# Optimization experiments

Measured on AMD Instinct MI355X. Metric: run time of the kernel, lower is better.

The kernel has to match this reference:

```python
import jax, jax.numpy as jnp
import numpy as np

EPS = 1e-5

def _bn(x, w, b, rm, rv):
    # eval-mode BatchNorm over channel axis (x: [..., C] broadcastable)
    return (x - rm) * (w * jax.lax.rsqrt(rv + EPS)) + b

def setup_inputs() -> dict:
    key = jax.random.key(0)
    ks = jax.random.split(key, 20)
    B, C, H, W = 2, 64, 96, 96
    Cq = C // 8  # query/key channels
    Cr = C // 8  # SE reduction channels
    s = 0.05
    inp = {
        'x': jax.random.normal(ks[0], (B, C, H, W), jnp.float32),
        'wq': jax.random.normal(ks[1], (Cq, C), jnp.float32) * s,
        'bq': jnp.zeros((Cq,), jnp.float32),
        'wk': jax.random.normal(ks[2], (Cq, C), jnp.float32) * s,
        'bk': jnp.zeros((Cq,), jnp.float32),
        'wv': jax.random.normal(ks[3], (C, C), jnp.float32) * s,
        'bv': jnp.zeros((C,), jnp.float32),
        'gamma': jnp.full((1,), 0.5, jnp.float32),
        'bn_w': jnp.ones((C,), jnp.float32),
        'bn_b': jnp.zeros((C,), jnp.float32),
        'bn_rm': jax.random.normal(ks[4], (C,), jnp.float32) * 0.1,
        'bn_rv': jax.random.uniform(ks[5], (C,), jnp.float32) + 0.5,
        'se_w1': jax.random.normal(ks[6], (Cr, C), jnp.float32) * s,
        'se_b1': jnp.zeros((Cr,), jnp.float32),
        'se_bn1_w': jnp.ones((Cr,), jnp.float32),
        'se_bn1_b': jnp.zeros((Cr,), jnp.float32),
        'se_bn1_rm': jax.random.normal(ks[7], (Cr,), jnp.float32) * 0.1,
        'se_bn1_rv': jax.random.uniform(ks[8], (Cr,), jnp.float32) + 0.5,
        'se_w2': jax.random.normal(ks[9], (C, Cr), jnp.float32) * s,
        'se_b2': jnp.zeros((C,), jnp.float32),
        'se_bn2_w': jnp.ones((C,), jnp.float32),
        'se_bn2_b': jnp.zeros((C,), jnp.float32),
        'se_bn2_rm': jax.random.normal(ks[10], (C,), jnp.float32) * 0.1,
        'se_bn2_rv': jax.random.uniform(ks[11], (C,), jnp.float32) + 0.5,
    }
    return inp

def reference(x, wq, bq, wk, bk, wv, bv, gamma, bn_w, bn_b, bn_rm, bn_rv,
              se_w1, se_b1, se_bn1_w, se_bn1_b, se_bn1_rm, se_bn1_rv,
              se_w2, se_b2, se_bn2_w, se_bn2_b, se_bn2_rm, se_bn2_rv):
    B, C, H, W = x.shape
    N = H * W
    xf = x.reshape(B, C, N)
    # PAM branch: 1x1 conv projections
    q = jnp.einsum('oc,bcn->bno', wq, xf) + bq            # [B,N,C/8]
    k = jnp.einsum('oc,bcn->bon', wk, xf) + bk[:, None]    # [B,C/8,N]
    v = jnp.einsum('oc,bcn->bon', wv, xf) + bv[:, None]    # [B,C,N]
    energy = jnp.einsum('bno,bom->bnm', q, k)              # [B,N,N]
    attn = jax.nn.softmax(energy, axis=-1)
    # out[b,c,i] = sum_j v[b,c,j] * attn[b,i,j]  (bmm(V, attn^T))
    out = jnp.einsum('bcj,bij->bci', v, attn)
    out = gamma[0] * out
    out = _bn(out, bn_w[:, None], bn_b[:, None], bn_rm[:, None], bn_rv[:, None])
    pam = out.reshape(B, C, H, W)
    # SE branch: GAP + 1x1 conv-bn-relu x2, multiplicative gate
    a = xf.mean(axis=2)                                    # [B,C]
    a1 = jax.nn.relu(_bn(a @ se_w1.T + se_b1, se_bn1_w, se_bn1_b, se_bn1_rm, se_bn1_rv))
    a2 = jax.nn.relu(_bn(a1 @ se_w2.T + se_b2, se_bn2_w, se_bn2_b, se_bn2_rm, se_bn2_rv))
    se = x * a2[:, :, None, None]
    return x + se + pam
```

## Files before the change

### kernel.cpp

```cpp
#include <hip/hip_runtime.h>
#include <hip/hip_bf16.h>

#define B_SZ   2
#define C_CH   64
#define NQ     8
#define NPIX   9216
#define NJC    288
#define QBLKS  288
#define KPART  8
#define KEYS_P 1152
#define NCHUNK 18
#define SM_F   2080
#define NP4    2304
#define KSTEP  (64*NQ)
#define VSTEP  4096

typedef short bf16x8 __attribute__((ext_vector_type(8)));
typedef float f32x4  __attribute__((ext_vector_type(4)));
typedef unsigned u32x4 __attribute__((ext_vector_type(4)));
typedef unsigned uint2v __attribute__((ext_vector_type(2)));

static __device__ __forceinline__ unsigned pack2bf(float a, float b){
    unsigned r;
    asm("v_cvt_pk_bf16_f32 %0, %1, %2" : "=v"(r) : "v"(a), "v"(b));
    return r;
}

__global__ __launch_bounds__(256) void prep_kernel(
    const float* __restrict__ x,
    const float* __restrict__ wq, const float* __restrict__ bq,
    const float* __restrict__ wk, const float* __restrict__ bk,
    const float* __restrict__ wv, const float* __restrict__ bv,
    __hip_bfloat16* __restrict__ qp, __hip_bfloat16* __restrict__ kp,
    __hip_bfloat16* __restrict__ vswz, float* __restrict__ amean)
{
    const int blk = blockIdx.x, tid = threadIdx.x;
    if (blk < 144){
        int t  = blk*256 + tid;
        int n  = (t % NP4) * 4;
        int c8 = (t / NP4) & 7;
        int b  = t / (NP4*8);
        c8 = __builtin_amdgcn_readfirstlane(c8);
        b  = __builtin_amdgcn_readfirstlane(b);
        float acc[8][4];
#pragma unroll
        for (int k = 0; k < 8; ++k){
            float bvv = bv[c8*8 + k];
            acc[k][0] = bvv; acc[k][1] = bvv; acc[k][2] = bvv; acc[k][3] = bvv;
        }
#pragma unroll 4
        for (int ci = 0; ci < C_CH; ++ci){
            const float4 xv = *reinterpret_cast<const float4*>(
                x + (size_t)(b*C_CH + ci)*NPIX + n);
#pragma unroll
            for (int k = 0; k < 8; ++k){
                float w = wv[(c8*8 + k)*C_CH + ci];
                acc[k][0] = fmaf(xv.x, w, acc[k][0]);
                acc[k][1] = fmaf(xv.y, w, acc[k][1]);
                acc[k][2] = fmaf(xv.z, w, acc[k][2]);
                acc[k][3] = fmaf(xv.w, w, acc[k][3]);
            }
        }
#pragma unroll
        for (int k = 0; k < 8; ++k){
            int c = c8*8 + k;
            size_t base = ((size_t)((b*NJC + (n >> 5))*4 + (c >> 4)))*512
                        + ((c & 15)*32) + (n & 31);
            unsigned long long wpk =
                (unsigned long long)pack2bf(acc[k][0], acc[k][1]) |
                ((unsigned long long)pack2bf(acc[k][2], acc[k][3]) << 32);
            *reinterpret_cast<unsigned long long*>(vswz + base) = wpk;
        }
    } else if (blk < 180){
        int t  = (blk - 144)*256 + tid;
        int n  = (t % NP4) * 4;
        int o8 = (t / NP4) & 1;
        int b  = t / (NP4*2);
        o8 = __builtin_amdgcn_readfirstlane(o8);
        b  = __builtin_amdgcn_readfirstlane(b);
        const bool isq = (o8 == 0);
        const float* w    = isq ? wq : wk;
        const float* bias = isq ? bq : bk;
        float acc[8][4];
#pragma unroll
        for (int k = 0; k < 8; ++k){
            float bb = bias[k];
            acc[k][0] = bb; acc[k][1] = bb; acc[k][2] = bb; acc[k][3] = bb;
        }
#pragma unroll 4
        for (int ci = 0; ci < C_CH; ++ci){
            const float4 xv = *reinterpret_cast<const float4*>(
                x + (size_t)(b*C_CH + ci)*NPIX + n);
#pragma unroll
            for (int k = 0; k < 8; ++k){
                float wv_ = w[k*C_CH + ci];
                acc[k][0] = fmaf(xv.x, wv_, acc[k][0]);
                acc[k][1] = fmaf(xv.y, wv_, acc[k][1]);
                acc[k][2] = fmaf(xv.z, wv_, acc[k][2]);
                acc[k][3] = fmaf(xv.w, wv_, acc[k][3]);
            }
        }
        if (isq){
#pragma unroll
            for (int k = 0; k < 8; ++k)
#pragma unroll
                for (int px = 0; px < 4; ++px) acc[k][px] *= 1.44269504f;
        }
        __hip_bfloat16* dst = isq ? qp : kp;
#pragma unroll
        for (int px = 0; px < 4; ++px){
            u32x4 row;
            row[0] = pack2bf(acc[0][px], acc[1][px]);
            row[1] = pack2bf(acc[2][px], acc[3][px]);
            row[2] = pack2bf(acc[4][px], acc[5][px]);
            row[3] = pack2bf(acc[6][px], acc[7][px]);
            *reinterpret_cast<u32x4*>(dst + ((size_t)(b*NPIX + n + px))*NQ) = row;
        }
    } else {
        int bc = blk - 180;
        float s = 0.f;
        for (int i = tid; i < NPIX; i += 256) s += x[(size_t)bc*NPIX + i];
#pragma unroll
        for (int o = 32; o > 0; o >>= 1) s += __shfl_down(s, o, 64);
        __shared__ float red[4];
        if ((tid & 63) == 0) red[tid >> 6] = s;
        __syncthreads();
        if (tid == 0) amean[bc] = (red[0] + red[1] + red[2] + red[3]) * (1.f / (float)NPIX);
    }
}

__global__ __launch_bounds__(512, 2) void flash_fused(
    const __hip_bfloat16* __restrict__ qp,
    const __hip_bfloat16* __restrict__ kp,
    const __hip_bfloat16* __restrict__ vswz,
    const float* __restrict__ amean,
    const float* __restrict__ sw1, const float* __restrict__ sb1,
    const float* __restrict__ s1w, const float* __restrict__ s1b,
    const float* __restrict__ s1m, const float* __restrict__ s1v,
    const float* __restrict__ sw2, const float* __restrict__ sb2,
    const float* __restrict__ s2w, const float* __restrict__ s2b,
    const float* __restrict__ s2m, const float* __restrict__ s2v,
    const float* __restrict__ x,
    const float* __restrict__ gamma,
    const float* __restrict__ bnw, const float* __restrict__ bnb,
    const float* __restrict__ bnm, const float* __restrict__ bnv,
    float* __restrict__ out)
{
    __shared__ __align__(16) float sm[4*SM_F];

    const int qt2 = blockIdx.x, b = blockIdx.y;
    const int p  = threadIdx.x >> 6;
    const int l  = threadIdx.x & 63;
    const int lq = l & 15;
    const int lg = l >> 4;
    const int vlane = lq*32 + lg*8;

    bf16x8 zf = {0,0,0,0,0,0,0,0};
    bf16x8 qfrag[2];
#pragma unroll
    for (int qi = 0; qi < 2; ++qi){
        qfrag[qi] = zf;
        if (lg == 0)
            qfrag[qi] = *reinterpret_cast<const bf16x8*>(
                qp + (size_t)(b*NPIX + qt2*32 + qi*16 + lq) * NQ);
    }

    bf16x8 ones;
#pragma unroll
    for (int i = 0; i < 8; ++i) ones[i] = (short)0x3F80;

    f32x4 Of[2][4];
#pragma unroll
    for (int qi = 0; qi < 2; ++qi)
#pragma unroll
        for (int i = 0; i < 4; ++i) Of[qi][i] = (f32x4){0.f, 0.f, 0.f, 0.f};
    f32x4 Lf[2];
    Lf[0] = (f32x4){0.f, 0.f, 0.f, 0.f};
    Lf[1] = (f32x4){0.f, 0.f, 0.f, 0.f};

    const __hip_bfloat16* kptr = kp + ((size_t)(b*NPIX + p*KEYS_P + lq))*NQ;
    const __hip_bfloat16* vptr = vswz + ((size_t)(b*NJC + p*(KEYS_P/32)))*4*512 + vlane;

    bf16x8 kfa[4], vfa[2][4];
    bf16x8 kfb[4], vfb[2][4];

    auto loadK = [&](bf16x8 (&dst)[4], const __hip_bfloat16* ptr){
#pragma unroll
        for (int jt = 0; jt < 4; ++jt){
            dst[jt] = zf;
            if (lg == 0)
                dst[jt] = *reinterpret_cast<const bf16x8*>(ptr + jt*16*NQ);
        }
    };
    auto loadV = [&](bf16x8 (&dst)[2][4], const __hip_bfloat16* ptr){
#pragma unroll
        for (int kc = 0; kc < 2; ++kc)
#pragma unroll
            for (int ct = 0; ct < 4; ++ct)
                dst[kc][ct] = *reinterpret_cast<const bf16x8*>(ptr + (kc*4 + ct)*512);
    };
    auto compute = [&](bf16x8 (&kfc)[4], bf16x8 (&vfc)[2][4]){
#pragma unroll
        for (int qi = 0; qi < 2; ++qi){
            f32x4 Sf[4];
#pragma unroll
            for (int jt = 0; jt < 4; ++jt)
                Sf[jt] = __builtin_amdgcn_mfma_f32_16x16x32_bf16(kfc[jt], qfrag[qi], (f32x4){0.f,0.f,0.f,0.f}, 0, 0, 0);
            unsigned D[4][2];
#pragma unroll
            for (int jt = 0; jt < 4; ++jt){
                D[jt][0] = pack2bf(exp2f(Sf[jt][0]), exp2f(Sf[jt][1]));
                D[jt][1] = pack2bf(exp2f(Sf[jt][2]), exp2f(Sf[jt][3]));
            }
#pragma unroll
            for (int kc = 0; kc < 2; ++kc){
                unsigned o0, o1, o2, o3;
                {
                    uint2v r1 = __builtin_amdgcn_permlane32_swap(D[2*kc][0], D[2*kc+1][0], false, false);
                    uint2v r2 = __builtin_amdgcn_permlane16_swap(r1[0], r1[1], false, false);
                    o0 = r2[0]; o2 = r2[1];
                }
                {
                    uint2v r1 = __builtin_amdgcn_permlane32_swap(D[2*kc][1], D[2*kc+1][1], false, false);
                    uint2v r2 = __builtin_amdgcn_permlane16_swap(r1[0], r1[1], false, false);
                    o1 = r2[0]; o3 = r2[1];
                }
                u32x4 pu; pu[0] = o0; pu[1] = o1; pu[2] = o2; pu[3] = o3;
                bf16x8 pf = __builtin_bit_cast(bf16x8, pu);
#pragma unroll
                for (int ct = 0; ct < 4; ++ct)
                    Of[qi][ct] = __builtin_amdgcn_mfma_f32_16x16x32_bf16(vfc[kc][ct], pf, Of[qi][ct], 0, 0, 0);
                Lf[qi] = __builtin_amdgcn_mfma_f32_16x16x32_bf16(ones, pf, Lf[qi], 0, 0, 0);
            }
        }
    };

    loadK(kfa, kptr); loadV(vfa, vptr);
    kptr += KSTEP; vptr += VSTEP;

    for (int it = 0; it < (NCHUNK - 2)/2; ++it){
        loadK(kfb, kptr); loadV(vfb, vptr);
        kptr += KSTEP; vptr += VSTEP;
        compute(kfa, vfa);
        loadK(kfa, kptr); loadV(vfa, vptr);
        kptr += KSTEP; vptr += VSTEP;
        compute(kfb, vfb);
    }
    loadK(kfb, kptr); loadV(vfb, vptr);
    compute(kfa, vfa);
    compute(kfb, vfb);

    float a1r;
    {
        int r8 = l & 7;
        float s = sb1[r8];
#pragma unroll 8
        for (int c = 0; c < C_CH; ++c)
            s = fmaf(amean[b*C_CH + c], sw1[r8*C_CH + c], s);
        s = (s - s1m[r8]) * (s1w[r8] * rsqrtf(s1v[r8] + 1e-5f)) + s1b[r8];
        a1r = fmaxf(s, 0.f);
    }

    if (p >= 4){
        const int ps = p - 4;
#pragma unroll
        for (int qi = 0; qi < 2; ++qi)
#pragma unroll
            for (int ct = 0; ct < 4; ++ct)
#pragma unroll
                for (int r = 0; r < 4; ++r)
                    sm[ps*SM_F + qi*1024 + (ct*4 + r)*64 + l] = Of[qi][ct][r];
        if (l < 16){
            sm[ps*SM_F + 2048 + lq]      = Lf[0][0];
            sm[ps*SM_F + 2048 + 16 + lq] = Lf[1][0];
        }
    }
    __syncthreads();
    if (p < 4){
#pragma unroll
        for (int qi = 0; qi < 2; ++qi)
#pragma unroll
            for (int ct = 0; ct < 4; ++ct)
#pragma unroll
                for (int r = 0; r < 4; ++r)
                    sm[p*SM_F + qi*1024 + (ct*4 + r)*64 + l] += Of[qi][ct][r];
        if (l < 16){
            sm[p*SM_F + 2048 + lq]      += Lf[0][0];
            sm[p*SM_F + 2048 + 16 + lq] += Lf[1][0];
        }
    }
    __syncthreads();

    {
        const int w8 = threadIdx.x >> 6;
        const int qi = w8 >> 2;
        const int ct = w8 & 3;
        float gam = gamma[0];

        float a1g[8];
#pragma unroll
        for (int j = 0; j < 8; ++j) a1g[j] = __shfl(a1r, (l & 56) | j, 64);
        float a2v[4];
#pragma unroll
        for (int r = 0; r < 4; ++r){
            int c = ct*16 + lg*4 + r;
            float s = sb2[c];
#pragma unroll
            for (int j = 0; j < 8; ++j) s = fmaf(a1g[j], sw2[c*NQ + j], s);
            s = (s - s2m[c]) * (s2w[c] * rsqrtf(s2v[c] + 1e-5f)) + s2b[c];
            a2v[r] = fmaxf(s, 0.f);
        }

        float L = 0.f;
#pragma unroll
        for (int q = 0; q < 4; ++q) L += sm[q*SM_F + 2048 + qi*16 + lq];
        float invL = 1.f / L;
        int n = qt2*32 + qi*16 + lq;
#pragma unroll
        for (int r = 0; r < 4; ++r){
            float O = 0.f;
#pragma unroll
            for (int q = 0; q < 4; ++q) O += sm[q*SM_F + qi*1024 + (ct*4 + r)*64 + l];
            int c = ct*16 + lg*4 + r;
            float pam = gam * O * invL;
            pam = (pam - bnm[c]) * (bnw[c] * rsqrtf(bnv[c] + 1e-5f)) + bnb[c];
            float xv = x[(size_t)(b*C_CH + c)*NPIX + n];
            out[(size_t)(b*C_CH + c)*NPIX + n] = fmaf(xv, a2v[r], xv + pam);
        }
    }
}

extern "C" void kernel_launch(void* const* d_in, const int* in_sizes, int n_in,
                              void* d_out, int out_size, void* d_ws, size_t ws_size,
                              hipStream_t stream)
{
    const float* x     = (const float*)d_in[0];
    const float* wq    = (const float*)d_in[1];
    const float* bq    = (const float*)d_in[2];
    const float* wk    = (const float*)d_in[3];
    const float* bk    = (const float*)d_in[4];
    const float* wv    = (const float*)d_in[5];
    const float* bv    = (const float*)d_in[6];
    const float* gamma = (const float*)d_in[7];
    const float* bnw   = (const float*)d_in[8];
    const float* bnb   = (const float*)d_in[9];
    const float* bnm   = (const float*)d_in[10];
    const float* bnv   = (const float*)d_in[11];
    const float* sw1   = (const float*)d_in[12];
    const float* sb1   = (const float*)d_in[13];
    const float* s1w   = (const float*)d_in[14];
    const float* s1b   = (const float*)d_in[15];
    const float* s1m   = (const float*)d_in[16];
    const float* s1v   = (const float*)d_in[17];
    const float* sw2   = (const float*)d_in[18];
    const float* sb2   = (const float*)d_in[19];
    const float* s2w   = (const float*)d_in[20];
    const float* s2b   = (const float*)d_in[21];
    const float* s2m   = (const float*)d_in[22];
    const float* s2v   = (const float*)d_in[23];

    size_t off = 0;
    auto give = [&](size_t bytes) -> void* {
        void* r = (char*)d_ws + off;
        off += (bytes + 255) & ~(size_t)255;
        return r;
    };
    __hip_bfloat16* qp   = (__hip_bfloat16*)give((size_t)B_SZ*NPIX*NQ*2);
    __hip_bfloat16* kp   = (__hip_bfloat16*)give((size_t)B_SZ*NPIX*NQ*2);
    __hip_bfloat16* vswz = (__hip_bfloat16*)give((size_t)B_SZ*C_CH*NPIX*2);
    float* amean = (float*)give((size_t)B_SZ*C_CH*4);

    prep_kernel<<<dim3(308), dim3(256), 0, stream>>>(x, wq, bq, wk, bk, wv, bv,
                                                     qp, kp, vswz, amean);
    flash_fused<<<dim3(QBLKS, B_SZ), dim3(512), 0, stream>>>(
        qp, kp, vswz, amean,
        sw1, sb1, s1w, s1b, s1m, s1v,
        sw2, sb2, s2w, s2b, s2m, s2v,
        x, gamma, bnw, bnb, bnm, bnv, (float*)d_out);
}
```

Before: 204.6 us.

## Switch flash attention to 32x32x16 MFMA with repacked K/V layouts

Replaces the 16x16x32 bf16 MFMA tiles in the fused attention kernel with 32x32x16 tiles. Q/K rows are padded to 16 channels with zeros, and V is reswizzled into 16-key by 32-channel blocks to match the new operand layout. A single permlane32 swap now replaces the permlane32+permlane16 pair, and the epilogue remaps LDS indices to the new accumulator layout. The K/V register double-buffering is simplified to prefetching only K while V is loaded inside each chunk. The launch bound of 2 blocks per CU is dropped. The intent is fewer MFMA issues and less wasted zero-padding per lane, at the cost of doubled Q/K storage, possible occupancy change and less V prefetch overlap.

Result: faster. 192.9 us (-5.8%).

```diff
diff --git a/kernel.cpp b/kernel.cpp
--- a/kernel.cpp
+++ b/kernel.cpp
@@ -4,19 +4,21 @@
 #define B_SZ   2
 #define C_CH   64
 #define NQ     8
+#define QKS    16
 #define NPIX   9216
-#define NJC    288
+#define NKS    576
 #define QBLKS  288
 #define KPART  8
 #define KEYS_P 1152
 #define NCHUNK 18
 #define SM_F   2080
 #define NP4    2304
-#define KSTEP  (64*NQ)
+#define KSTEP2 1024
 #define VSTEP  4096
 
 typedef short bf16x8 __attribute__((ext_vector_type(8)));
 typedef float f32x4  __attribute__((ext_vector_type(4)));
+typedef float f32x16 __attribute__((ext_vector_type(16)));
 typedef unsigned u32x4 __attribute__((ext_vector_type(4)));
 typedef unsigned uint2v __attribute__((ext_vector_type(2)));
 
@@ -64,8 +66,8 @@
 #pragma unroll
         for (int k = 0; k < 8; ++k){
             int c = c8*8 + k;
-            size_t base = ((size_t)((b*NJC + (n >> 5))*4 + (c >> 4)))*512
-                        + ((c & 15)*32) + (n & 31);
+            size_t base = ((size_t)((b*NKS + (n >> 4))*2 + (c >> 5)))*512
+                        + (((n >> 3) & 1) << 8) + ((c & 31) << 3) + (n & 7);
             unsigned long long wpk =
                 (unsigned long long)pack2bf(acc[k][0], acc[k][1]) |
                 ((unsigned long long)pack2bf(acc[k][2], acc[k][3]) << 32);
@@ -107,6 +109,7 @@
                 for (int px = 0; px < 4; ++px) acc[k][px] *= 1.44269504f;
         }
         __hip_bfloat16* dst = isq ? qp : kp;
+        u32x4 zr; zr[0] = 0; zr[1] = 0; zr[2] = 0; zr[3] = 0;
 #pragma unroll
         for (int px = 0; px < 4; ++px){
             u32x4 row;
@@ -114,7 +117,9 @@
             row[1] = pack2bf(acc[2][px], acc[3][px]);
             row[2] = pack2bf(acc[4][px], acc[5][px]);
             row[3] = pack2bf(acc[6][px], acc[7][px]);
-            *reinterpret_cast<u32x4*>(dst + ((size_t)(b*NPIX + n + px))*NQ) = row;
+            __hip_bfloat16* d0 = dst + ((size_t)(b*NPIX + n + px))*QKS;
+            *reinterpret_cast<u32x4*>(d0)     = row;
+            *reinterpret_cast<u32x4*>(d0 + 8) = zr;
         }
     } else {
         int bc = blk - 180;
@@ -129,7 +134,7 @@
     }
 }
 
-__global__ __launch_bounds__(512, 2) void flash_fused(
+__global__ __launch_bounds__(512) void flash_fused(
     const __hip_bfloat16* __restrict__ qp,
     const __hip_bfloat16* __restrict__ kp,
     const __hip_bfloat16* __restrict__ vswz,
@@ -151,104 +156,77 @@
     const int qt2 = blockIdx.x, b = blockIdx.y;
     const int p  = threadIdx.x >> 6;
     const int l  = threadIdx.x & 63;
-    const int lq = l & 15;
-    const int lg = l >> 4;
-    const int vlane = lq*32 + lg*8;
-
-    bf16x8 zf = {0,0,0,0,0,0,0,0};
-    bf16x8 qfrag[2];
-#pragma unroll
-    for (int qi = 0; qi < 2; ++qi){
-        qfrag[qi] = zf;
-        if (lg == 0)
-            qfrag[qi] = *reinterpret_cast<const bf16x8*>(
-                qp + (size_t)(b*NPIX + qt2*32 + qi*16 + lq) * NQ);
-    }
+    const int lc = l & 31;
+    const int lh = l >> 5;
+
+    bf16x8 qfrag = *reinterpret_cast<const bf16x8*>(
+        qp + ((size_t)(b*NPIX + qt2*32 + lc))*QKS + lh*8);
 
     bf16x8 ones;
 #pragma unroll
     for (int i = 0; i < 8; ++i) ones[i] = (short)0x3F80;
 
-    f32x4 Of[2][4];
-#pragma unroll
-    for (int qi = 0; qi < 2; ++qi)
-#pragma unroll
-        for (int i = 0; i < 4; ++i) Of[qi][i] = (f32x4){0.f, 0.f, 0.f, 0.f};
-    f32x4 Lf[2];
-    Lf[0] = (f32x4){0.f, 0.f, 0.f, 0.f};
-    Lf[1] = (f32x4){0.f, 0.f, 0.f, 0.f};
-
-    const __hip_bfloat16* kptr = kp + ((size_t)(b*NPIX + p*KEYS_P + lq))*NQ;
-    const __hip_bfloat16* vptr = vswz + ((size_t)(b*NJC + p*(KEYS_P/32)))*4*512 + vlane;
-
-    bf16x8 kfa[4], vfa[2][4];
-    bf16x8 kfb[4], vfb[2][4];
-
-    auto loadK = [&](bf16x8 (&dst)[4], const __hip_bfloat16* ptr){
-#pragma unroll
-        for (int jt = 0; jt < 4; ++jt){
-            dst[jt] = zf;
-            if (lg == 0)
-                dst[jt] = *reinterpret_cast<const bf16x8*>(ptr + jt*16*NQ);
+    f32x16 zero16;
+#pragma unroll
+    for (int i = 0; i < 16; ++i) zero16[i] = 0.f;
+
+    f32x16 Of0 = zero16, Of1 = zero16;
+    f32x16 Lacc = zero16;
+
+    const __hip_bfloat16* kptr = kp + ((size_t)(b*NPIX + p*KEYS_P + lc))*QKS + lh*8;
+    const __hip_bfloat16* vptr = vswz + ((size_t)((b*NKS + p*(KEYS_P/16))*2))*512 + l*8;
+
+    auto CHUNK = [&](const bf16x8& k0, const bf16x8& k1){
+        bf16x8 vf[8];
+#pragma unroll
+        for (int t = 0; t < 8; ++t)
+            vf[t] = *reinterpret_cast<const bf16x8*>(vptr + t*512);
+        vptr += VSTEP;
+
+        unsigned D[16];
+#pragma unroll
+        for (int kt = 0; kt < 2; ++kt){
+            f32x16 s = __builtin_amdgcn_mfma_f32_32x32x16_bf16(
+                kt ? k1 : k0, qfrag, zero16, 0, 0, 0);
+#pragma unroll
+            for (int g = 0; g < 4; ++g){
+                float e0 = exp2f(s[4*g+0]), e1 = exp2f(s[4*g+1]);
+                float e2 = exp2f(s[4*g+2]), e3 = exp2f(s[4*g+3]);
+                D[kt*8 + g*2 + 0] = pack2bf(e0, e1);
+                D[kt*8 + g*2 + 1] = pack2bf(e2, e3);
+            }
+        }
+#pragma unroll
+        for (int ks = 0; ks < 4; ++ks){
+            const int base = (ks >> 1)*8 + (ks & 1)*4;
+            uint2v r0 = __builtin_amdgcn_permlane32_swap(D[base+0], D[base+2], false, false);
+            uint2v r1 = __builtin_amdgcn_permlane32_swap(D[base+1], D[base+3], false, false);
+            u32x4 pu; pu[0] = r0[0]; pu[1] = r1[0]; pu[2] = r0[1]; pu[3] = r1[1];
+            bf16x8 pf = __builtin_bit_cast(bf16x8, pu);
+            Of0  = __builtin_amdgcn_mfma_f32_32x32x16_bf16(vf[ks*2+0], pf, Of0, 0, 0, 0);
+            Of1  = __builtin_amdgcn_mfma_f32_32x32x16_bf16(vf[ks*2+1], pf, Of1, 0, 0, 0);
+            Lacc = __builtin_amdgcn_mfma_f32_32x32x16_bf16(ones,       pf, Lacc, 0, 0, 0);
         }
     };
-    auto loadV = [&](bf16x8 (&dst)[2][4], const __hip_bfloat16* ptr){
-#pragma unroll
-        for (int kc = 0; kc < 2; ++kc)
-#pragma unroll
-            for (int ct = 0; ct < 4; ++ct)
-                dst[kc][ct] = *reinterpret_cast<const bf16x8*>(ptr + (kc*4 + ct)*512);
-    };
-    auto compute = [&](bf16x8 (&kfc)[4], bf16x8 (&vfc)[2][4]){
-#pragma unroll
-        for (int qi = 0; qi < 2; ++qi){
-            f32x4 Sf[4];
-#pragma unroll
-            for (int jt = 0; jt < 4; ++jt)
-                Sf[jt] = __builtin_amdgcn_mfma_f32_16x16x32_bf16(kfc[jt], qfrag[qi], (f32x4){0.f,0.f,0.f,0.f}, 0, 0, 0);
-            unsigned D[4][2];
-#pragma unroll
-            for (int jt = 0; jt < 4; ++jt){
-                D[jt][0] = pack2bf(exp2f(Sf[jt][0]), exp2f(Sf[jt][1]));
-                D[jt][1] = pack2bf(exp2f(Sf[jt][2]), exp2f(Sf[jt][3]));
-            }
-#pragma unroll
-            for (int kc = 0; kc < 2; ++kc){
-                unsigned o0, o1, o2, o3;
-                {
-                    uint2v r1 = __builtin_amdgcn_permlane32_swap(D[2*kc][0], D[2*kc+1][0], false, false);
-                    uint2v r2 = __builtin_amdgcn_permlane16_swap(r1[0], r1[1], false, false);
-                    o0 = r2[0]; o2 = r2[1];
-                }
-                {
-                    uint2v r1 = __builtin_amdgcn_permlane32_swap(D[2*kc][1], D[2*kc+1][1], false, false);
-                    uint2v r2 = __builtin_amdgcn_permlane16_swap(r1[0], r1[1], false, false);
-                    o1 = r2[0]; o3 = r2[1];
-                }
-                u32x4 pu; pu[0] = o0; pu[1] = o1; pu[2] = o2; pu[3] = o3;
-                bf16x8 pf = __builtin_bit_cast(bf16x8, pu);
-#pragma unroll
-                for (int ct = 0; ct < 4; ++ct)
-                    Of[qi][ct] = __builtin_amdgcn_mfma_f32_16x16x32_bf16(vfc[kc][ct], pf, Of[qi][ct], 0, 0, 0);
-                Lf[qi] = __builtin_amdgcn_mfma_f32_16x16x32_bf16(ones, pf, Lf[qi], 0, 0, 0);
-            }
-        }
-    };
-
-    loadK(kfa, kptr); loadV(vfa, vptr);
-    kptr += KSTEP; vptr += VSTEP;
-
+
+    bf16x8 kA0 = *reinterpret_cast<const bf16x8*>(kptr);
+    bf16x8 kA1 = *reinterpret_cast<const bf16x8*>(kptr + 512);
+    kptr += KSTEP2;
+    bf16x8 kB0, kB1;
     for (int it = 0; it < (NCHUNK - 2)/2; ++it){
-        loadK(kfb, kptr); loadV(vfb, vptr);
-        kptr += KSTEP; vptr += VSTEP;
-        compute(kfa, vfa);
-        loadK(kfa, kptr); loadV(vfa, vptr);
-        kptr += KSTEP; vptr += VSTEP;
-        compute(kfb, vfb);
-    }
-    loadK(kfb, kptr); loadV(vfb, vptr);
-    compute(kfa, vfa);
-    compute(kfb, vfb);
+        kB0 = *reinterpret_cast<const bf16x8*>(kptr);
+        kB1 = *reinterpret_cast<const bf16x8*>(kptr + 512);
+        kptr += KSTEP2;
+        CHUNK(kA0, kA1);
+        kA0 = *reinterpret_cast<const bf16x8*>(kptr);
+        kA1 = *reinterpret_cast<const bf16x8*>(kptr + 512);
+        kptr += KSTEP2;
+        CHUNK(kB0, kB1);
+    }
+    kB0 = *reinterpret_cast<const bf16x8*>(kptr);
+    kB1 = *reinterpret_cast<const bf16x8*>(kptr + 512);
+    CHUNK(kA0, kA1);
+    CHUNK(kB0, kB1);
 
     float a1r;
     {
@@ -264,37 +242,27 @@
     if (p >= 4){
         const int ps = p - 4;
 #pragma unroll
-        for (int qi = 0; qi < 2; ++qi)
-#pragma unroll
-            for (int ct = 0; ct < 4; ++ct)
-#pragma unroll
-                for (int r = 0; r < 4; ++r)
-                    sm[ps*SM_F + qi*1024 + (ct*4 + r)*64 + l] = Of[qi][ct][r];
-        if (l < 16){
-            sm[ps*SM_F + 2048 + lq]      = Lf[0][0];
-            sm[ps*SM_F + 2048 + 16 + lq] = Lf[1][0];
-        }
+        for (int r = 0; r < 16; ++r){
+            sm[ps*SM_F +        r*64 + l] = Of0[r];
+            sm[ps*SM_F + 1024 + r*64 + l] = Of1[r];
+        }
+        if (l < 32) sm[ps*SM_F + 2048 + l] = Lacc[0];
     }
     __syncthreads();
     if (p < 4){
 #pragma unroll
-        for (int qi = 0; qi < 2; ++qi)
-#pragma unroll
-            for (int ct = 0; ct < 4; ++ct)
-#pragma unroll
-                for (int r = 0; r < 4; ++r)
-                    sm[p*SM_F + qi*1024 + (ct*4 + r)*64 + l] += Of[qi][ct][r];
-        if (l < 16){
-            sm[p*SM_F + 2048 + lq]      += Lf[0][0];
-            sm[p*SM_F + 2048 + 16 + lq] += Lf[1][0];
-        }
+        for (int r = 0; r < 16; ++r){
+            sm[p*SM_F +        r*64 + l] += Of0[r];
+            sm[p*SM_F + 1024 + r*64 + l] += Of1[r];
+        }
+        if (l < 32) sm[p*SM_F + 2048 + l] += Lacc[0];
     }
     __syncthreads();
 
     {
         const int w8 = threadIdx.x >> 6;
-        const int qi = w8 >> 2;
-        const int ct = w8 & 3;
+        const int i  = lc;
+        const int cg = w8*2 + lh;
         float gam = gamma[0];
 
         float a1g[8];
@@ -303,7 +271,7 @@
         float a2v[4];
 #pragma unroll
         for (int r = 0; r < 4; ++r){
-            int c = ct*16 + lg*4 + r;
+            int c = cg*4 + r;
             float s = sb2[c];
 #pragma unroll
             for (int j = 0; j < 8; ++j) s = fmaf(a1g[j], sw2[c*NQ + j], s);
@@ -313,15 +281,19 @@
 
         float L = 0.f;
 #pragma unroll
-        for (int q = 0; q < 4; ++q) L += sm[q*SM_F + 2048 + qi*16 + lq];
+        for (int q = 0; q < 4; ++q) L += sm[q*SM_F + 2048 + i];
         float invL = 1.f / L;
-        int n = qt2*32 + qi*16 + lq;
+        int n = qt2*32 + i;
 #pragma unroll
         for (int r = 0; r < 4; ++r){
+            int c = cg*4 + r;
+            int c5   = c & 31;
+            int reg  = (c5 & 3) + 4*(c5 >> 3);
+            int lsrc = (c5 >> 2) & 1;
+            int o    = (c >> 5)*1024 + reg*64 + lsrc*32 + i;
             float O = 0.f;
 #pragma unroll
-            for (int q = 0; q < 4; ++q) O += sm[q*SM_F + qi*1024 + (ct*4 + r)*64 + l];
-            int c = ct*16 + lg*4 + r;
+            for (int q = 0; q < 4; ++q) O += sm[q*SM_F + o];
             float pam = gam * O * invL;
             pam = (pam - bnm[c]) * (bnw[c] * rsqrtf(bnv[c] + 1e-5f)) + bnb[c];
             float xv = x[(size_t)(b*C_CH + c)*NPIX + n];
@@ -365,8 +337,8 @@
         off += (bytes + 255) & ~(size_t)255;
         return r;
     };
-    __hip_bfloat16* qp   = (__hip_bfloat16*)give((size_t)B_SZ*NPIX*NQ*2);
-    __hip_bfloat16* kp   = (__hip_bfloat16*)give((size_t)B_SZ*NPIX*NQ*2);
+    __hip_bfloat16* qp   = (__hip_bfloat16*)give((size_t)B_SZ*NPIX*QKS*2);
+    __hip_bfloat16* kp   = (__hip_bfloat16*)give((size_t)B_SZ*NPIX*QKS*2);
     __hip_bfloat16* vswz = (__hip_bfloat16*)give((size_t)B_SZ*C_CH*NPIX*2);
     float* amean = (float*)give((size_t)B_SZ*C_CH*4);
 
```
